# Kernel tuning notes

Measured on AMD Instinct MI355X. Metric: run time of the kernel, lower is better.

The kernel has to match this reference:

```python
import jax, jax.numpy as jnp
import numpy as np

D_MODEL = 1024
NUM_HEADS = 16
HEAD_DIM = D_MODEL // NUM_HEADS


def setup_inputs() -> dict:
    key = jax.random.key(0)
    kq, kk, kv, kw, kb = jax.random.split(key, 5)
    N, S = 2, 2048
    query = jax.random.normal(kq, (N, S, D_MODEL), dtype=jnp.float32)
    key_t = jax.random.normal(kk, (N, S, D_MODEL), dtype=jnp.float32)
    value = jax.random.normal(kv, (N, S, D_MODEL), dtype=jnp.float32)
    # fc_out params (nn.Linear(d_model, d_model)): W [out,in], b [out]
    lim = 1.0 / np.sqrt(D_MODEL)
    W_out = jax.random.uniform(kw, (D_MODEL, D_MODEL), minval=-lim, maxval=lim, dtype=jnp.float32)
    b_out = jax.random.uniform(kb, (D_MODEL,), minval=-lim, maxval=lim, dtype=jnp.float32)
    return {"query": query, "key": key_t, "value": value, "W_out": W_out, "b_out": b_out}


def reference(query, key, value, W_out, b_out):
    N, Lq, _ = query.shape
    Lk = key.shape[1]
    q = query.reshape(N, Lq, NUM_HEADS, HEAD_DIM)
    k = key.reshape(N, Lk, NUM_HEADS, HEAD_DIM)
    v = value.reshape(N, Lk, NUM_HEADS, HEAD_DIM)
    # NOTE: original module does NOT apply q/k/v Linear layers and does NOT scale by 1/sqrt(d)
    scores = jnp.einsum("nqhd,nkhd->nhqk", q, k)
    attn = jax.nn.softmax(scores, axis=3)
    out = jnp.einsum("nhqk,nkhd->nqhd", attn, v).reshape(N, Lq, D_MODEL)
    return out @ W_out.T + b_out
```

## Files before the change

### kernel.cpp

```cpp
#include <hip/hip_runtime.h>

typedef _Float16 half8 __attribute__((ext_vector_type(8)));
typedef _Float16 half4 __attribute__((ext_vector_type(4)));
typedef float f32x4 __attribute__((ext_vector_type(4)));
typedef float f32x16 __attribute__((ext_vector_type(16)));
typedef unsigned u32x4 __attribute__((ext_vector_type(4)));

#define N_B 2
#define S_LEN 2048
#define NH 16
#define HD 64
#define DM 1024
#define LOG2E 1.44269504088896f

__device__ __forceinline__ void gload16(const void* g, void* l) {
    __builtin_amdgcn_global_load_lds(
        (const __attribute__((address_space(1))) unsigned int*)g,
        (__attribute__((address_space(3))) unsigned int*)l, 16, 0, 0);
}

__device__ __forceinline__ float fexp2(float x) {
    float r;
    asm("v_exp_f32 %0, %1" : "=v"(r) : "v"(x));
    return r;
}

__global__ __launch_bounds__(256) void k_prep(const float* __restrict__ K,
                                              const float* __restrict__ V,
                                              const float* __restrict__ Wo,
                                              _Float16* __restrict__ Kh,
                                              _Float16* __restrict__ Vt,
                                              _Float16* __restrict__ Wh) {
    __shared__ _Float16 tile[64][65];
    const int id = blockIdx.x;
    if (id < 4096) {
        int i = id * 256 + threadIdx.x;
        float4 v = ((const float4*)K)[i];
        int base = i * 4;
        int d = base & 63;
        int h = (base >> 6) & 15;
        int s = (base >> 10) & 2047;
        int n = base >> 21;
        size_t o = ((size_t)((n * NH + h) * S_LEN + s)) * HD + d;
        half4 hv = {(_Float16)v.x, (_Float16)v.y, (_Float16)v.z, (_Float16)v.w};
        *(half4*)(Kh + o) = hv;
    } else if (id < 5120) {
        int b = id - 4096;
        int st = b & 31, h = (b >> 5) & 15, n = b >> 9;
        int c = threadIdx.x & 63, r0 = threadIdx.x >> 6;
#pragma unroll
        for (int i = 0; i < 16; ++i) {
            int r = i * 4 + r0;
            tile[r][c] = (_Float16)V[((size_t)(n * S_LEN) + st * 64 + r) * DM + h * HD + c];
        }
        __syncthreads();
#pragma unroll
        for (int i = 0; i < 16; ++i) {
            int d = i * 4 + r0;
            Vt[((size_t)((n * NH + h) * HD + d)) * S_LEN + st * 64 + c] = tile[c][d];
        }
    } else {
        int i = (id - 5120) * 256 + threadIdx.x;
        float4 v = ((const float4*)Wo)[i];
        half4 hv = {(_Float16)v.x, (_Float16)v.y, (_Float16)v.z, (_Float16)v.w};
        *(half4*)(Wh + (size_t)i * 4) = hv;
    }
}

__global__ __launch_bounds__(512, 4) void k_attn(const float* __restrict__ Q,
                                                 const _Float16* __restrict__ Kh,
                                                 const _Float16* __restrict__ Vth,
                                                 _Float16* __restrict__ Oatt) {
    __shared__ char SB[49152];

    const int id = blockIdx.x;
    const int xcd = id & 7;
    const int sl = id >> 3;
    const int nh = xcd + 8 * (sl >> 4);
    const int qt = sl & 15;

    const int tid = threadIdx.x;
    const int w = tid >> 6;
    const int wq = w & 3;
    const int hf = w >> 2;
    const int lane = tid & 63;
    const int l31 = lane & 31;
    const int hi = lane >> 5;
    const int n = nh >> 4, h = nh & 15;

    const size_t head = (size_t)nh * S_LEN * HD;
    const char* Khead = (const char*)(Kh + head);
    const char* Vhead = (const char*)(Vth + head);

    const int qg = qt * 128 + wq * 32 + l31;
    const float* qbase = Q + ((size_t)(n * S_LEN) + qg) * DM + h * HD;
    auto mkqf = [&](int c) -> half8 {
        float4 a = *(const float4*)(qbase + 16 * c + 8 * hi);
        float4 b = *(const float4*)(qbase + 16 * c + 8 * hi + 4);
        half8 r = {(_Float16)(a.x * LOG2E), (_Float16)(a.y * LOG2E),
                   (_Float16)(a.z * LOG2E), (_Float16)(a.w * LOG2E),
                   (_Float16)(b.x * LOG2E), (_Float16)(b.y * LOG2E),
                   (_Float16)(b.z * LOG2E), (_Float16)(b.w * LOG2E)};
        return r;
    };
    half8 qf0 = mkqf(0), qf1 = mkqf(1), qf2 = mkqf(2), qf3 = mkqf(3);

    f32x16 oacc0 = {}, oacc1 = {};
    float m_q = -1e30f, l_q = 0.f;

    const int rr = lane >> 3;
    const int cb = (lane & 7) * 16;
    const int gcb = cb ^ (rr << 4);

    auto kbuf = [&](int b, int half) -> char* { return SB + (b * 2 + half) * 8192; };
    auto vbuf = [&](int half) -> char* { return SB + 32768 + half * 8192; };

    auto STAGE_K = [&](int t, int b) {
#pragma unroll
        for (int j = 0; j < 2; ++j) {
            int slice = wq * 2 + j;
            int row = slice * 8 + rr;
            int key = hf * 1024 + t * 64 + row;
            gload16(Khead + (size_t)key * 128 + gcb, kbuf(b, hf) + slice * 1024);
        }
    };
    auto STAGE_V = [&](int t) {
#pragma unroll
        for (int j = 0; j < 2; ++j) {
            int slice = wq * 2 + j;
            int row = slice * 8 + rr;
            gload16(Vhead + (size_t)row * 4096 + hf * 2048 + t * 128 + gcb,
                    vbuf(hf) + slice * 1024);
        }
    };

    const int rmask = (l31 & 7) << 4;
    auto ldF = [&](const char* lds, int blk, int c) -> half8 {
        int off = (32 * blk + l31) * 128 + ((32 * c + 16 * hi) ^ rmask);
        return *(const half8*)(lds + off);
    };

    auto pk2 = [&](float a, float b) -> unsigned {
        unsigned short ua = __builtin_bit_cast(unsigned short, (_Float16)a);
        unsigned short ub = __builtin_bit_cast(unsigned short, (_Float16)b);
        return (unsigned)ua | ((unsigned)ub << 16);
    };
    auto mkpa = [&](const f32x16& S, int rb) -> half8 {
        unsigned w0 = pk2(S[rb + 0], S[rb + 1]);
        unsigned w1 = pk2(S[rb + 2], S[rb + 3]);
        unsigned w2 = pk2(S[rb + 4], S[rb + 5]);
        unsigned w3 = pk2(S[rb + 6], S[rb + 7]);
        unsigned x0 = (unsigned)__shfl_xor((int)w0, 32);
        unsigned x1 = (unsigned)__shfl_xor((int)w1, 32);
        unsigned x2 = (unsigned)__shfl_xor((int)w2, 32);
        unsigned x3 = (unsigned)__shfl_xor((int)w3, 32);
        u32x4 t;
        t[0] = hi ? x2 : w0;
        t[1] = hi ? x3 : w1;
        t[2] = hi ? w2 : x0;
        t[3] = hi ? w3 : x1;
        return __builtin_bit_cast(half8, t);
    };

    STAGE_K(0, 0);
    __syncthreads();

    for (int t = 0; t < 16; ++t) {
        const int buf = t & 1;
        STAGE_V(t);
        if (t < 15) STAGE_K(t + 1, buf ^ 1);
        const char* ldsK = kbuf(buf, hf);

        f32x16 s0 = {}, s1 = {};
        __builtin_amdgcn_s_setprio(1);
        s0 = __builtin_amdgcn_mfma_f32_32x32x16_f16(ldF(ldsK, 0, 0), qf0, s0, 0, 0, 0);
        s0 = __builtin_amdgcn_mfma_f32_32x32x16_f16(ldF(ldsK, 0, 1), qf1, s0, 0, 0, 0);
        s0 = __builtin_amdgcn_mfma_f32_32x32x16_f16(ldF(ldsK, 0, 2), qf2, s0, 0, 0, 0);
        s0 = __builtin_amdgcn_mfma_f32_32x32x16_f16(ldF(ldsK, 0, 3), qf3, s0, 0, 0, 0);
        s1 = __builtin_amdgcn_mfma_f32_32x32x16_f16(ldF(ldsK, 1, 0), qf0, s1, 0, 0, 0);
        s1 = __builtin_amdgcn_mfma_f32_32x32x16_f16(ldF(ldsK, 1, 1), qf1, s1, 0, 0, 0);
        s1 = __builtin_amdgcn_mfma_f32_32x32x16_f16(ldF(ldsK, 1, 2), qf2, s1, 0, 0, 0);
        s1 = __builtin_amdgcn_mfma_f32_32x32x16_f16(ldF(ldsK, 1, 3), qf3, s1, 0, 0, 0);
        __builtin_amdgcn_s_setprio(0);

        float mx[16];
#pragma unroll
        for (int i = 0; i < 16; ++i) mx[i] = fmaxf(s0[i], s1[i]);
#pragma unroll
        for (int st = 8; st > 0; st >>= 1)
#pragma unroll
            for (int i = 0; i < 8; ++i)
                if (i < st) mx[i] = fmaxf(mx[i], mx[i + st]);
        float tm = fmaxf(mx[0], __shfl_xor(mx[0], 32));
        if (!__all(tm <= m_q + 8.f)) {
            float mn = fmaxf(m_q, tm);
            float sc = fexp2(m_q - mn);
            m_q = mn;
            l_q *= sc;
            int scb = __builtin_bit_cast(int, sc);
#pragma unroll
            for (int r = 0; r < 16; ++r) {
                int qr = (r & 3) + 8 * (r >> 2) + 4 * hi;
                float s = __builtin_bit_cast(float, __builtin_amdgcn_ds_bpermute(4 * qr, scb));
                oacc0[r] *= s;
                oacc1[r] *= s;
            }
        }
        float rs = 0.f;
#pragma unroll
        for (int i = 0; i < 16; ++i) { float p = fexp2(s0[i] - m_q); s0[i] = p; rs += p; }
#pragma unroll
        for (int i = 0; i < 16; ++i) { float p = fexp2(s1[i] - m_q); s1[i] = p; rs += p; }
        rs += __shfl_xor(rs, 32);
        l_q += rs;

        half8 pa0 = mkpa(s0, 0), pa1 = mkpa(s0, 8);
        half8 pa2 = mkpa(s1, 0), pa3 = mkpa(s1, 8);

        __syncthreads();

        const char* ldsV = vbuf(hf);
        __builtin_amdgcn_s_setprio(1);
        oacc0 = __builtin_amdgcn_mfma_f32_32x32x16_f16(pa0, ldF(ldsV, 0, 0), oacc0, 0, 0, 0);
        oacc0 = __builtin_amdgcn_mfma_f32_32x32x16_f16(pa1, ldF(ldsV, 0, 1), oacc0, 0, 0, 0);
        oacc0 = __builtin_amdgcn_mfma_f32_32x32x16_f16(pa2, ldF(ldsV, 0, 2), oacc0, 0, 0, 0);
        oacc0 = __builtin_amdgcn_mfma_f32_32x32x16_f16(pa3, ldF(ldsV, 0, 3), oacc0, 0, 0, 0);
        oacc1 = __builtin_amdgcn_mfma_f32_32x32x16_f16(pa0, ldF(ldsV, 1, 0), oacc1, 0, 0, 0);
        oacc1 = __builtin_amdgcn_mfma_f32_32x32x16_f16(pa1, ldF(ldsV, 1, 1), oacc1, 0, 0, 0);
        oacc1 = __builtin_amdgcn_mfma_f32_32x32x16_f16(pa2, ldF(ldsV, 1, 2), oacc1, 0, 0, 0);
        oacc1 = __builtin_amdgcn_mfma_f32_32x32x16_f16(pa3, ldF(ldsV, 1, 3), oacc1, 0, 0, 0);
        __builtin_amdgcn_s_setprio(0);

        __syncthreads();
    }

    float* MRG = (float*)SB;
    if (hf == 1) {
        float* B = MRG + wq * 2176;
        B[lane] = m_q;
        B[64 + lane] = l_q;
#pragma unroll
        for (int r = 0; r < 16; ++r) {
            B[128 + r * 64 + lane] = oacc0[r];
            B[1152 + r * 64 + lane] = oacc1[r];
        }
    }
    __syncthreads();
    if (hf == 0) {
        float* B = MRG + wq * 2176;
        float m1 = B[lane], l1 = B[64 + lane];
        float m = fmaxf(m_q, m1);
        float e0 = fexp2(m_q - m), e1 = fexp2(m1 - m);
        float linv = 1.f / (l_q * e0 + l1 * e1);
        int e0b = __builtin_bit_cast(int, e0);
        int e1b = __builtin_bit_cast(int, e1);
        int ivb = __builtin_bit_cast(int, linv);
#pragma unroll
        for (int r = 0; r < 16; ++r) {
            int qr = (r & 3) + 8 * (r >> 2) + 4 * hi;
            float s0f = __builtin_bit_cast(float, __builtin_amdgcn_ds_bpermute(4 * qr, e0b));
            float s1f = __builtin_bit_cast(float, __builtin_amdgcn_ds_bpermute(4 * qr, e1b));
            float iv = __builtin_bit_cast(float, __builtin_amdgcn_ds_bpermute(4 * qr, ivb));
            float o0 = (oacc0[r] * s0f + B[128 + r * 64 + lane] * s1f) * iv;
            float o1 = (oacc1[r] * s0f + B[1152 + r * 64 + lane] * s1f) * iv;
            int qglob = qt * 128 + wq * 32 + qr;
            size_t base = ((size_t)(n * S_LEN + qglob)) * DM + h * HD + l31;
            Oatt[base] = (_Float16)o0;
            Oatt[base + 32] = (_Float16)o1;
        }
    }
}

__global__ __launch_bounds__(256) void k_proj(const _Float16* __restrict__ A,
                                              const _Float16* __restrict__ W,
                                              const float* __restrict__ bias,
                                              float* __restrict__ out) {
    __shared__ _Float16 As[2][128 * 64];
    __shared__ _Float16 Ws[2][128 * 64];

    const int id = blockIdx.x;
    const int ot = id & 7;
    const int mt = id >> 3;
    const int tid = threadIdx.x;
    const int w = tid >> 6;
    const int lane = tid & 63;
    const int lr = lane & 15, lg = lane >> 4;
    const int wm = (w >> 1) * 64, wn = (w & 1) * 64;

    const int rr = lane >> 3;
    const int cb = (lane & 7) * 16;
    const int gcb = cb ^ (rr << 4);

    const char* Abase = (const char*)(A + (size_t)(mt * 128) * DM);
    const char* Wbase = (const char*)(W + (size_t)(ot * 128) * DM);

    auto STAGE = [&](int kt, int b) {
#pragma unroll
        for (int r = 0; r < 4; ++r) {
            int row = r * 32 + w * 8 + rr;
            gload16(Abase + (size_t)row * 2048 + kt * 128 + gcb,
                    (char*)&As[b][0] + (r * 32 + w * 8) * 128);
            gload16(Wbase + (size_t)row * 2048 + kt * 128 + gcb,
                    (char*)&Ws[b][0] + (r * 32 + w * 8) * 128);
        }
    };

    f32x4 zero = {0.f, 0.f, 0.f, 0.f};
    f32x4 acc[4][4];
#pragma unroll
    for (int mi = 0; mi < 4; ++mi)
#pragma unroll
        for (int ni = 0; ni < 4; ++ni) acc[mi][ni] = zero;

    auto COMPUTE = [&](int b) {
        const char* ldsA = (const char*)&As[b][0];
        const char* ldsW = (const char*)&Ws[b][0];
        half8 af[4][2], wf[4][2];
#pragma unroll
        for (int mi = 0; mi < 4; ++mi) {
            int row = wm + mi * 16 + lr;
            int sw = (row & 7) << 4;
            const char* p = ldsA + row * 128;
            af[mi][0] = *(const half8*)(p + ((lg * 16) ^ sw));
            af[mi][1] = *(const half8*)(p + ((64 + lg * 16) ^ sw));
        }
#pragma unroll
        for (int ni = 0; ni < 4; ++ni) {
            int row = wn + ni * 16 + lr;
            int sw = (row & 7) << 4;
            const char* p = ldsW + row * 128;
            wf[ni][0] = *(const half8*)(p + ((lg * 16) ^ sw));
            wf[ni][1] = *(const half8*)(p + ((64 + lg * 16) ^ sw));
        }
#pragma unroll
        for (int mi = 0; mi < 4; ++mi)
#pragma unroll
            for (int ni = 0; ni < 4; ++ni) {
                acc[mi][ni] = __builtin_amdgcn_mfma_f32_16x16x32_f16(af[mi][0], wf[ni][0], acc[mi][ni], 0, 0, 0);
                acc[mi][ni] = __builtin_amdgcn_mfma_f32_16x16x32_f16(af[mi][1], wf[ni][1], acc[mi][ni], 0, 0, 0);
            }
    };

    STAGE(0, 0);
    __syncthreads();
    for (int kt = 0; kt < 15; ++kt) {
        STAGE(kt + 1, (kt & 1) ^ 1);
        COMPUTE(kt & 1);
        __syncthreads();
    }
    COMPUTE(1);

#pragma unroll
    for (int ni = 0; ni < 4; ++ni) {
        int o = ot * 128 + wn + ni * 16 + lr;
        float b = bias[o];
#pragma unroll
        for (int mi = 0; mi < 4; ++mi)
#pragma unroll
            for (int i = 0; i < 4; ++i) {
                int m = mt * 128 + wm + mi * 16 + lg * 4 + i;
                out[(size_t)m * DM + o] = acc[mi][ni][i] + b;
            }
    }
}

extern "C" void kernel_launch(void* const* d_in, const int* in_sizes, int n_in,
                              void* d_out, int out_size, void* d_ws, size_t ws_size,
                              hipStream_t stream) {
    const float* Q = (const float*)d_in[0];
    const float* K = (const float*)d_in[1];
    const float* V = (const float*)d_in[2];
    const float* Wo = (const float*)d_in[3];
    const float* bo = (const float*)d_in[4];
    float* out = (float*)d_out;
    char* ws = (char*)d_ws;

    _Float16* Kh = (_Float16*)(ws);
    _Float16* Vt = (_Float16*)(ws + (8u << 20));
    _Float16* Oatt = (_Float16*)(ws + (16u << 20));
    _Float16* Wh = (_Float16*)(ws + (24u << 20));

    k_prep<<<6144, 256, 0, stream>>>(K, V, Wo, Kh, Vt, Wh);
    k_attn<<<512, 512, 0, stream>>>(Q, Kh, Vt, Oatt);
    k_proj<<<256, 256, 0, stream>>>(Oatt, Wh, bo, out);
}
```

Baseline: 99.22 us.

## Load K/V fragments directly from global memory instead of LDS staging

Removes the async global-to-LDS double-buffered staging of K and V tiles and the per-iteration block barriers. Each wave now reads its MFMA operand fragments straight from global memory into registers. It also shortens the row-max reduction by deferring the cross-half shuffle into the rescale branch, raises the rescale threshold, and moves the row-sum shuffle out of the loop. The cost is that every wave re-reads K/V from global/L2 instead of sharing through LDS, and load latency is no longer hidden by prefetch.

```diff
diff --git a/kernel.cpp b/kernel.cpp
--- a/kernel.cpp
+++ b/kernel.cpp
@@ -71,7 +71,7 @@
                                                  const _Float16* __restrict__ Kh,
                                                  const _Float16* __restrict__ Vth,
                                                  _Float16* __restrict__ Oatt) {
-    __shared__ char SB[49152];
+    __shared__ float MRG[4 * 2176];
 
     const int id = blockIdx.x;
     const int xcd = id & 7;
@@ -108,37 +108,8 @@
     f32x16 oacc0 = {}, oacc1 = {};
     float m_q = -1e30f, l_q = 0.f;
 
-    const int rr = lane >> 3;
-    const int cb = (lane & 7) * 16;
-    const int gcb = cb ^ (rr << 4);
-
-    auto kbuf = [&](int b, int half) -> char* { return SB + (b * 2 + half) * 8192; };
-    auto vbuf = [&](int half) -> char* { return SB + 32768 + half * 8192; };
-
-    auto STAGE_K = [&](int t, int b) {
-#pragma unroll
-        for (int j = 0; j < 2; ++j) {
-            int slice = wq * 2 + j;
-            int row = slice * 8 + rr;
-            int key = hf * 1024 + t * 64 + row;
-            gload16(Khead + (size_t)key * 128 + gcb, kbuf(b, hf) + slice * 1024);
-        }
-    };
-    auto STAGE_V = [&](int t) {
-#pragma unroll
-        for (int j = 0; j < 2; ++j) {
-            int slice = wq * 2 + j;
-            int row = slice * 8 + rr;
-            gload16(Vhead + (size_t)row * 4096 + hf * 2048 + t * 128 + gcb,
-                    vbuf(hf) + slice * 1024);
-        }
-    };
-
-    const int rmask = (l31 & 7) << 4;
-    auto ldF = [&](const char* lds, int blk, int c) -> half8 {
-        int off = (32 * blk + l31) * 128 + ((32 * c + 16 * hi) ^ rmask);
-        return *(const half8*)(lds + off);
-    };
+    const char* kbase = Khead + ((size_t)(hf * 1024 + l31)) * 128 + 16 * hi;
+    const char* vbase = Vhead + (size_t)l31 * 4096 + hf * 2048 + 16 * hi;
 
     auto pk2 = [&](float a, float b) -> unsigned {
         unsigned short ua = __builtin_bit_cast(unsigned short, (_Float16)a);
@@ -162,37 +133,39 @@
         return __builtin_bit_cast(half8, t);
     };
 
-    STAGE_K(0, 0);
-    __syncthreads();
-
     for (int t = 0; t < 16; ++t) {
-        const int buf = t & 1;
-        STAGE_V(t);
-        if (t < 15) STAGE_K(t + 1, buf ^ 1);
-        const char* ldsK = kbuf(buf, hf);
+        const char* kt0 = kbase + t * 8192;
+        half8 kf[2][4];
+#pragma unroll
+        for (int blk = 0; blk < 2; ++blk)
+#pragma unroll
+            for (int c = 0; c < 4; ++c)
+                kf[blk][c] = *(const half8*)(kt0 + blk * 4096 + c * 32);
 
         f32x16 s0 = {}, s1 = {};
         __builtin_amdgcn_s_setprio(1);
-        s0 = __builtin_amdgcn_mfma_f32_32x32x16_f16(ldF(ldsK, 0, 0), qf0, s0, 0, 0, 0);
-        s0 = __builtin_amdgcn_mfma_f32_32x32x16_f16(ldF(ldsK, 0, 1), qf1, s0, 0, 0, 0);
-        s0 = __builtin_amdgcn_mfma_f32_32x32x16_f16(ldF(ldsK, 0, 2), qf2, s0, 0, 0, 0);
-        s0 = __builtin_amdgcn_mfma_f32_32x32x16_f16(ldF(ldsK, 0, 3), qf3, s0, 0, 0, 0);
-        s1 = __builtin_amdgcn_mfma_f32_32x32x16_f16(ldF(ldsK, 1, 0), qf0, s1, 0, 0, 0);
-        s1 = __builtin_amdgcn_mfma_f32_32x32x16_f16(ldF(ldsK, 1, 1), qf1, s1, 0, 0, 0);
-        s1 = __builtin_amdgcn_mfma_f32_32x32x16_f16(ldF(ldsK, 1, 2), qf2, s1, 0, 0, 0);
-        s1 = __builtin_amdgcn_mfma_f32_32x32x16_f16(ldF(ldsK, 1, 3), qf3, s1, 0, 0, 0);
+        s0 = __builtin_amdgcn_mfma_f32_32x32x16_f16(kf[0][0], qf0, s0, 0, 0, 0);
+        s0 = __builtin_amdgcn_mfma_f32_32x32x16_f16(kf[0][1], qf1, s0, 0, 0, 0);
+        s0 = __builtin_amdgcn_mfma_f32_32x32x16_f16(kf[0][2], qf2, s0, 0, 0, 0);
+        s0 = __builtin_amdgcn_mfma_f32_32x32x16_f16(kf[0][3], qf3, s0, 0, 0, 0);
+        s1 = __builtin_amdgcn_mfma_f32_32x32x16_f16(kf[1][0], qf0, s1, 0, 0, 0);
+        s1 = __builtin_amdgcn_mfma_f32_32x32x16_f16(kf[1][1], qf1, s1, 0, 0, 0);
+        s1 = __builtin_amdgcn_mfma_f32_32x32x16_f16(kf[1][2], qf2, s1, 0, 0, 0);
+        s1 = __builtin_amdgcn_mfma_f32_32x32x16_f16(kf[1][3], qf3, s1, 0, 0, 0);
         __builtin_amdgcn_s_setprio(0);
 
-        float mx[16];
-#pragma unroll
-        for (int i = 0; i < 16; ++i) mx[i] = fmaxf(s0[i], s1[i]);
-#pragma unroll
-        for (int st = 8; st > 0; st >>= 1)
-#pragma unroll
-            for (int i = 0; i < 8; ++i)
-                if (i < st) mx[i] = fmaxf(mx[i], mx[i + st]);
-        float tm = fmaxf(mx[0], __shfl_xor(mx[0], 32));
-        if (!__all(tm <= m_q + 8.f)) {
+        float a0 = fmaxf(fmaxf(s0[0], s0[1]), fmaxf(s0[2], s0[3]));
+        float a1 = fmaxf(fmaxf(s0[4], s0[5]), fmaxf(s0[6], s0[7]));
+        float a2 = fmaxf(fmaxf(s0[8], s0[9]), fmaxf(s0[10], s0[11]));
+        float a3 = fmaxf(fmaxf(s0[12], s0[13]), fmaxf(s0[14], s0[15]));
+        float b0 = fmaxf(fmaxf(s1[0], s1[1]), fmaxf(s1[2], s1[3]));
+        float b1 = fmaxf(fmaxf(s1[4], s1[5]), fmaxf(s1[6], s1[7]));
+        float b2 = fmaxf(fmaxf(s1[8], s1[9]), fmaxf(s1[10], s1[11]));
+        float b3 = fmaxf(fmaxf(s1[12], s1[13]), fmaxf(s1[14], s1[15]));
+        float lmax = fmaxf(fmaxf(fmaxf(a0, a1), fmaxf(a2, a3)),
+                           fmaxf(fmaxf(b0, b1), fmaxf(b2, b3)));
+        if (!__all(lmax <= m_q + 14.f)) {
+            float tm = fmaxf(lmax, __shfl_xor(lmax, 32));
             float mn = fmaxf(m_q, tm);
             float sc = fexp2(m_q - mn);
             m_q = mn;
@@ -206,35 +179,54 @@
                 oacc1[r] *= s;
             }
         }
-        float rs = 0.f;
-#pragma unroll
-        for (int i = 0; i < 16; ++i) { float p = fexp2(s0[i] - m_q); s0[i] = p; rs += p; }
-#pragma unroll
-        for (int i = 0; i < 16; ++i) { float p = fexp2(s1[i] - m_q); s1[i] = p; rs += p; }
-        rs += __shfl_xor(rs, 32);
-        l_q += rs;
+        float r0 = 0.f, r1 = 0.f, r2 = 0.f, r3 = 0.f;
+#pragma unroll
+        for (int i = 0; i < 16; i += 4) {
+            float p0 = fexp2(s0[i + 0] - m_q); s0[i + 0] = p0; r0 += p0;
+            float p1 = fexp2(s0[i + 1] - m_q); s0[i + 1] = p1; r1 += p1;
+            float p2 = fexp2(s0[i + 2] - m_q); s0[i + 2] = p2; r2 += p2;
+            float p3 = fexp2(s0[i + 3] - m_q); s0[i + 3] = p3; r3 += p3;
+        }
+#pragma unroll
+        for (int i = 0; i < 16; i += 4) {
+            float p0 = fexp2(s1[i + 0] - m_q); s1[i + 0] = p0; r0 += p0;
+            float p1 = fexp2(s1[i + 1] - m_q); s1[i + 1] = p1; r1 += p1;
+            float p2 = fexp2(s1[i + 2] - m_q); s1[i + 2] = p2; r2 += p2;
+            float p3 = fexp2(s1[i + 3] - m_q); s1[i + 3] = p3; r3 += p3;
+        }
+        l_q += (r0 + r1) + (r2 + r3);
 
         half8 pa0 = mkpa(s0, 0), pa1 = mkpa(s0, 8);
         half8 pa2 = mkpa(s1, 0), pa3 = mkpa(s1, 8);
 
-        __syncthreads();
-
-        const char* ldsV = vbuf(hf);
-        __builtin_amdgcn_s_setprio(1);
-        oacc0 = __builtin_amdgcn_mfma_f32_32x32x16_f16(pa0, ldF(ldsV, 0, 0), oacc0, 0, 0, 0);
-        oacc0 = __builtin_amdgcn_mfma_f32_32x32x16_f16(pa1, ldF(ldsV, 0, 1), oacc0, 0, 0, 0);
-        oacc0 = __builtin_amdgcn_mfma_f32_32x32x16_f16(pa2, ldF(ldsV, 0, 2), oacc0, 0, 0, 0);
-        oacc0 = __builtin_amdgcn_mfma_f32_32x32x16_f16(pa3, ldF(ldsV, 0, 3), oacc0, 0, 0, 0);
-        oacc1 = __builtin_amdgcn_mfma_f32_32x32x16_f16(pa0, ldF(ldsV, 1, 0), oacc1, 0, 0, 0);
-        oacc1 = __builtin_amdgcn_mfma_f32_32x32x16_f16(pa1, ldF(ldsV, 1, 1), oacc1, 0, 0, 0);
-        oacc1 = __builtin_amdgcn_mfma_f32_32x32x16_f16(pa2, ldF(ldsV, 1, 2), oacc1, 0, 0, 0);
-        oacc1 = __builtin_amdgcn_mfma_f32_32x32x16_f16(pa3, ldF(ldsV, 1, 3), oacc1, 0, 0, 0);
-        __builtin_amdgcn_s_setprio(0);
-
-        __syncthreads();
-    }
-
-    float* MRG = (float*)SB;
+        {
+            const char* vt0 = vbase + t * 128;
+            half8 v0 = *(const half8*)(vt0 + 0);
+            half8 v1 = *(const half8*)(vt0 + 32);
+            half8 v2 = *(const half8*)(vt0 + 64);
+            half8 v3 = *(const half8*)(vt0 + 96);
+            __builtin_amdgcn_s_setprio(1);
+            oacc0 = __builtin_amdgcn_mfma_f32_32x32x16_f16(pa0, v0, oacc0, 0, 0, 0);
+            oacc0 = __builtin_amdgcn_mfma_f32_32x32x16_f16(pa1, v1, oacc0, 0, 0, 0);
+            oacc0 = __builtin_amdgcn_mfma_f32_32x32x16_f16(pa2, v2, oacc0, 0, 0, 0);
+            oacc0 = __builtin_amdgcn_mfma_f32_32x32x16_f16(pa3, v3, oacc0, 0, 0, 0);
+            __builtin_amdgcn_s_setprio(0);
+            const char* vt1 = vt0 + 131072;
+            half8 u0 = *(const half8*)(vt1 + 0);
+            half8 u1 = *(const half8*)(vt1 + 32);
+            half8 u2 = *(const half8*)(vt1 + 64);
+            half8 u3 = *(const half8*)(vt1 + 96);
+            __builtin_amdgcn_s_setprio(1);
+            oacc1 = __builtin_amdgcn_mfma_f32_32x32x16_f16(pa0, u0, oacc1, 0, 0, 0);
+            oacc1 = __builtin_amdgcn_mfma_f32_32x32x16_f16(pa1, u1, oacc1, 0, 0, 0);
+            oacc1 = __builtin_amdgcn_mfma_f32_32x32x16_f16(pa2, u2, oacc1, 0, 0, 0);
+            oacc1 = __builtin_amdgcn_mfma_f32_32x32x16_f16(pa3, u3, oacc1, 0, 0, 0);
+            __builtin_amdgcn_s_setprio(0);
+        }
+    }
+
+    l_q += __shfl_xor(l_q, 32);
+
     if (hf == 1) {
         float* B = MRG + wq * 2176;
         B[lane] = m_q;
```

Result: slower. 158.0 us (+59.3%).
